# Kernel tuning notes

Measured on AMD Instinct MI355X. Metric: run time of the kernel, lower is better.

## Reference

```python
import jax, jax.numpy as jnp
import numpy as np

SOS = 0
MAX_LENGTH = 64

N_LATENTS = 256
N_CHARACTERS = 128
N_HIDDENS = 1024
BATCH = 4096


def setup_inputs() -> dict:
    key = jax.random.key(0)
    ks = jax.random.split(key, 16)
    H, L, C = N_HIDDENS, N_LATENTS, N_CHARACTERS
    s = 0.02
    return {
        "z": jax.random.normal(ks[0], (BATCH, L), dtype=jnp.float32),
        "embed_w": jax.random.normal(ks[1], (C, H), dtype=jnp.float32) * s,
        "z2h_w": jax.random.normal(ks[2], (H, L), dtype=jnp.float32) * s,
        "z2h_b": jnp.zeros((H,), dtype=jnp.float32),
        "w_ih0": jax.random.normal(ks[3], (3 * H, H + L), dtype=jnp.float32) * s,
        "w_hh0": jax.random.normal(ks[4], (3 * H, H), dtype=jnp.float32) * s,
        "b_ih0": jnp.zeros((3 * H,), dtype=jnp.float32),
        "b_hh0": jnp.zeros((3 * H,), dtype=jnp.float32),
        "w_ih1": jax.random.normal(ks[5], (3 * H, H), dtype=jnp.float32) * s,
        "w_hh1": jax.random.normal(ks[6], (3 * H, H), dtype=jnp.float32) * s,
        "b_ih1": jnp.zeros((3 * H,), dtype=jnp.float32),
        "b_hh1": jnp.zeros((3 * H,), dtype=jnp.float32),
        "h2o_w": jax.random.normal(ks[7], (C, H + L), dtype=jnp.float32) * s,
        "h2o_b": jnp.zeros((C,), dtype=jnp.float32),
    }


def _gru_cell(x, h, w_ih, w_hh, b_ih, b_hh):
    # PyTorch GRUCell math. x: [B, I], h: [B, H]
    gi = x @ w_ih.T + b_ih  # [B, 3H]
    gh = h @ w_hh.T + b_hh  # [B, 3H]
    i_r, i_z, i_n = jnp.split(gi, 3, axis=1)
    h_r, h_z, h_n = jnp.split(gh, 3, axis=1)
    r = jax.nn.sigmoid(i_r + h_r)
    zg = jax.nn.sigmoid(i_z + h_z)
    n = jnp.tanh(i_n + r * h_n)
    return (1.0 - zg) * n + zg * h


def reference(z, embed_w, z2h_w, z2h_b,
              w_ih0, w_hh0, b_ih0, b_hh0,
              w_ih1, w_hh1, b_ih1, b_hh1,
              h2o_w, h2o_b):
    batch = z.shape[0]
    h0 = z @ z2h_w.T + z2h_b  # [B, H], replicated across both GRU layers

    def step(carry, _):
        c_in, h1, h2 = carry
        e = embed_w[c_in]                      # [B, H] embedding lookup
        e = e * jax.nn.sigmoid(e)              # swish
        x = jnp.concatenate([e, z], axis=1)    # [B, H+L]
        h1 = _gru_cell(x, h1, w_ih0, w_hh0, b_ih0, b_hh0)
        h2 = _gru_cell(h1, h2, w_ih1, w_hh1, b_ih1, b_hh1)
        out = jnp.concatenate([h2, z], axis=1) @ h2o_w.T + h2o_b  # [B, C]
        # argmax(log_softmax(out)) == argmax(out)
        sample = jnp.argmax(out, axis=1).astype(jnp.int32)
        return (sample, h1, h2), out

    c0 = jnp.full((batch,), SOS, dtype=jnp.int32)
    _, outs = jax.lax.scan(step, (c0, h0, h0), None, length=MAX_LENGTH)
    return jnp.transpose(outs, (1, 0, 2))  # [B, T, C]
```

## Files before the change

kernel.cpp:

```cpp
#include <hip/hip_runtime.h>
#include <hip/hip_bf16.h>
#include <stdint.h>
#include <stddef.h>

#define B_   4096
#define H_   1024
#define L_   256
#define C_   128
#define T_   64
#define H3_  3072

typedef unsigned short u16;
typedef __attribute__((ext_vector_type(8))) short bf16x8;
typedef __attribute__((ext_vector_type(4))) float f32x4;

typedef const void __attribute__((address_space(1)))* as1_cvp;
typedef void __attribute__((address_space(3)))* as3_vp;

__device__ __forceinline__ void gl2lds16(const void* g, void* l) {
  __builtin_amdgcn_global_load_lds((as1_cvp)g, (as3_vp)l, 16, 0, 0);
}

__device__ __forceinline__ float bf2f(u16 u) {
  union { float f; unsigned int i; } x; x.i = ((unsigned int)u) << 16; return x.f;
}
__device__ __forceinline__ u16 f2bf(float f) {
  union { float f; unsigned int i; } x; x.f = f;
  unsigned int r = x.i + 0x7fffu + ((x.i >> 16) & 1u);
  return (u16)(r >> 16);
}
__device__ __forceinline__ float sigm(float x) { return 1.f / (1.f + __expf(-x)); }
__device__ __forceinline__ float tanh_fast(float x) {
  float e = __expf(2.f * x); return 1.f - 2.f / (e + 1.f);
}

template<int OUT_MODE>
__device__ __forceinline__ void gemm_tile_body(
    u16* As, u16* Ws,
    const u16* __restrict__ A, int lda,
    const u16* __restrict__ W, int ldw,
    const float* __restrict__ bias,
    void* __restrict__ C0p, void* __restrict__ C1p, int ldc, int K,
    int m0, int n0)
{
  const int tid  = threadIdx.x;
  const int wave = tid >> 6, lane = tid & 63;
  const int wm = (wave >> 1) * 64, wn = (wave & 1) * 64;
  const int lrow = lane & 15, lq = lane >> 4;
  const int arow = wave * 8 + (lane >> 3);
  const int acol = (lane & 7) * 8;

  f32x4 acc[4][4] = {};

  const u16* Ag = A + (size_t)m0 * lda;
  const u16* Wg = W + (size_t)n0 * ldw;

  for (int k0 = 0; k0 < K; k0 += 64) {
    __syncthreads();
    #pragma unroll
    for (int rd = 0; rd < 4; rd++) {
      gl2lds16(Ag + (size_t)(rd * 32 + arow) * lda + (k0 + acol), As + rd * 2048 + wave * 512);
      gl2lds16(Wg + (size_t)(rd * 32 + arow) * ldw + (k0 + acol), Ws + rd * 2048 + wave * 512);
    }
    __syncthreads();
    #pragma unroll
    for (int kk = 0; kk < 64; kk += 32) {
      bf16x8 af[4], bw[4];
      #pragma unroll
      for (int i = 0; i < 4; i++)
        af[i] = *(const bf16x8*)&As[(wm + i * 16 + lrow) * 64 + kk + lq * 8];
      #pragma unroll
      for (int j = 0; j < 4; j++)
        bw[j] = *(const bf16x8*)&Ws[(wn + j * 16 + lrow) * 64 + kk + lq * 8];
      #pragma unroll
      for (int i = 0; i < 4; i++)
        #pragma unroll
        for (int j = 0; j < 4; j++)
          acc[i][j] = __builtin_amdgcn_mfma_f32_16x16x32_bf16(af[i], bw[j], acc[i][j], 0, 0, 0);
    }
  }

  #pragma unroll
  for (int j = 0; j < 4; j++) {
    const int col = n0 + wn + j * 16 + lrow;
    const float bv = bias ? bias[col] : 0.f;
    #pragma unroll
    for (int i = 0; i < 4; i++) {
      #pragma unroll
      for (int r = 0; r < 4; r++) {
        const int row = m0 + wm + i * 16 + lq * 4 + r;
        float v = acc[i][j][r] + bv;
        if (OUT_MODE == 0) {
          ((float*)C0p)[(size_t)row * ldc + col] = v;
        } else if (OUT_MODE == 1) {
          ((u16*)C0p)[(size_t)row * ldc + col] = f2bf(v);
        } else {
          u16 hv = f2bf(v);
          ((u16*)C0p)[(size_t)row * ldc + col] = hv;
          ((u16*)C1p)[(size_t)row * ldc + col] = hv;
        }
      }
    }
  }
}

template<int OUT_MODE>
__global__ __launch_bounds__(256) void gemm_bt(
    const u16* __restrict__ A, int lda,
    const u16* __restrict__ W, int ldw,
    const float* __restrict__ bias,
    void* __restrict__ C0p, void* __restrict__ C1p, int ldc, int K)
{
  __shared__ __align__(16) u16 As[128 * 64];
  __shared__ __align__(16) u16 Ws[128 * 64];
  gemm_tile_body<OUT_MODE>(As, Ws, A, lda, W, ldw, bias, C0p, C1p, ldc, K,
                           blockIdx.y * 128, blockIdx.x * 128);
}

__device__ __forceinline__ void out_body(
    u16* As, u16* Ws, int ob,
    const u16* __restrict__ h2, const u16* __restrict__ Wo,
    const float* __restrict__ Oz, float* __restrict__ outp,
    int* __restrict__ cnew, int t)
{
  const int tid = threadIdx.x, wave = tid >> 6, lane = tid & 63;
  const int b0 = ob * 64;
  const int lrow = lane & 15, lq = lane >> 4;
  const int arow = wave * 8 + (lane >> 3);
  const int acol = (lane & 7) * 8;
  f32x4 acc[8] = {};

  for (int k0 = 0; k0 < H_; k0 += 64) {
    __syncthreads();
    #pragma unroll
    for (int rd = 0; rd < 2; rd++)
      gl2lds16(h2 + (size_t)(b0 + rd * 32 + arow) * H_ + k0 + acol, As + rd * 2048 + wave * 512);
    #pragma unroll
    for (int rd = 0; rd < 4; rd++)
      gl2lds16(Wo + (size_t)(rd * 32 + arow) * H_ + k0 + acol, Ws + rd * 2048 + wave * 512);
    __syncthreads();
    #pragma unroll
    for (int kk = 0; kk < 64; kk += 32) {
      bf16x8 af = *(const bf16x8*)&As[(wave * 16 + lrow) * 64 + kk + lq * 8];
      #pragma unroll
      for (int j = 0; j < 8; j++) {
        bf16x8 bw = *(const bf16x8*)&Ws[(j * 16 + lrow) * 64 + kk + lq * 8];
        acc[j] = __builtin_amdgcn_mfma_f32_16x16x32_bf16(af, bw, acc[j], 0, 0, 0);
      }
    }
  }

  #pragma unroll
  for (int r = 0; r < 4; r++) {
    const int row = b0 + wave * 16 + lq * 4 + r;
    float mv = -3.4e38f; int mi = 0;
    #pragma unroll
    for (int j = 0; j < 8; j++) {
      const int col = j * 16 + lrow;
      float v = acc[j][r] + Oz[(size_t)row * C_ + col];
      outp[(size_t)row * (T_ * C_) + t * C_ + col] = v;
      if (v > mv) { mv = v; mi = col; }
    }
    #pragma unroll
    for (int off = 1; off < 16; off <<= 1) {
      float ov = __shfl_xor(mv, off);
      int   oi = __shfl_xor(mi, off);
      if (ov > mv || (ov == mv && oi < mi)) { mv = ov; mi = oi; }
    }
    if (lrow == 0) cnew[row] = mi;
  }
}

__global__ __launch_bounds__(256) void out_k(
    const u16* __restrict__ h2cur, const u16* __restrict__ Wo,
    const float* __restrict__ Oz, float* __restrict__ outp,
    int* __restrict__ cbuf, int t)
{
  __shared__ __align__(16) u16 As[64 * 64];
  __shared__ __align__(16) u16 Ws[128 * 64];
  out_body(As, Ws, blockIdx.x, h2cur, Wo, Oz, outp, cbuf, t);
}


#define A_TSZ 16384
#define W_TSZ 12288

__device__ __forceinline__ void stageA_lo(const u16* Ag, int k0, u16* bA) {
  const int tid = threadIdx.x, wave = tid >> 6, lane = tid & 63;
  const int r64 = wave * 8 + (lane >> 3);
  const int cSw = (((lane & 7) ^ ((lane >> 5) << 1)) << 3);
  gl2lds16(Ag + (size_t)(r64) * H_ + k0 + cSw, bA + wave * 512);
  gl2lds16(Ag + (size_t)(64 + r64) * H_ + k0 + cSw, bA + 4096 + wave * 512);
}
__device__ __forceinline__ void stageA_hi(const u16* Ag, int k0, u16* bA) {
  const int tid = threadIdx.x, wave = tid >> 6, lane = tid & 63;
  const int r64 = wave * 8 + (lane >> 3);
  const int cSw = (((lane & 7) ^ ((lane >> 5) << 1)) << 3);
  gl2lds16(Ag + (size_t)(128 + r64) * H_ + k0 + cSw, bA + 8192 + wave * 512);
  gl2lds16(Ag + (size_t)(192 + r64) * H_ + k0 + cSw, bA + 12288 + wave * 512);
}
__device__ __forceinline__ void stageW(const u16* Wg, int k0, u16* bW) {
  const int tid = threadIdx.x, wave = tid >> 6, lane = tid & 63;
  const int r64 = wave * 8 + (lane >> 3);
  const int cSw = (((lane & 7) ^ ((lane >> 5) << 1)) << 3);
  #pragma unroll
  for (int rd = 0; rd < 3; rd++)
    gl2lds16(Wg + (size_t)(rd * 1024 + r64) * H_ + k0 + cSw, bW + rd * 4096 + wave * 512);
}

template<int PHASE>
__device__ __forceinline__ void phase_reads(const u16* bA, const u16* bW,
    bf16x8 af0[4], bf16x8 af1[4], bf16x8 bwv[2][2])
{
  const int tid = threadIdx.x, wave = tid >> 6, lane = tid & 63;
  const int wmh = wave >> 1, wj = wave & 1;
  const int lrow = lane & 15, lq = lane >> 4;
  const int rsw = ((lrow >> 2) & 1) << 4;
  const int c0 = (lq * 8) ^ rsw;
  const int c1 = (32 + lq * 8) ^ rsw;
  if (PHASE == 0) {
    #pragma unroll
    for (int i = 0; i < 4; i++)
      af0[i] = *(const bf16x8*)&bA[(wmh * 64 + i * 16 + lrow) * 64 + c0];
    #pragma unroll
    for (int u = 0; u < 2; u++) {
      bwv[0][u] = *(const bf16x8*)&bW[(wj * 32 + u * 16 + lrow) * 64 + c0];
      bwv[1][u] = *(const bf16x8*)&bW[(64 + wj * 32 + u * 16 + lrow) * 64 + c0];
    }
  } else if (PHASE == 1) {
    #pragma unroll
    for (int i = 0; i < 4; i++)
      af1[i] = *(const bf16x8*)&bA[(wmh * 64 + i * 16 + lrow) * 64 + c1];
    #pragma unroll
    for (int u = 0; u < 2; u++) {
      bwv[0][u] = *(const bf16x8*)&bW[(128 + wj * 32 + u * 16 + lrow) * 64 + c0];
      bwv[1][u] = *(const bf16x8*)&bW[(wj * 32 + u * 16 + lrow) * 64 + c1];
    }
  } else {
    #pragma unroll
    for (int u = 0; u < 2; u++) {
      bwv[0][u] = *(const bf16x8*)&bW[(64 + wj * 32 + u * 16 + lrow) * 64 + c1];
      bwv[1][u] = *(const bf16x8*)&bW[(128 + wj * 32 + u * 16 + lrow) * 64 + c1];
    }
  }
}

template<int PHASE, bool PH2v>
__device__ __forceinline__ void phase_fma(const bf16x8 bwv[2][2],
    const bf16x8 af0[4], const bf16x8 af1[4],
    f32x4 acc[3][2][4], f32x4 accN[2][4])
{
  if (PHASE == 0) {
    #pragma unroll
    for (int u = 0; u < 2; u++)
      #pragma unroll
      for (int i = 0; i < 4; i++) {
        acc[0][u][i] = __builtin_amdgcn_mfma_f32_16x16x32_bf16(af0[i], bwv[0][u], acc[0][u][i], 0, 0, 0);
        acc[1][u][i] = __builtin_amdgcn_mfma_f32_16x16x32_bf16(af0[i], bwv[1][u], acc[1][u][i], 0, 0, 0);
      }
  } else if (PHASE == 1) {
    #pragma unroll
    for (int u = 0; u < 2; u++)
      #pragma unroll
      for (int i = 0; i < 4; i++) {
        if (PH2v)
          accN[u][i] = __builtin_amdgcn_mfma_f32_16x16x32_bf16(af0[i], bwv[0][u], accN[u][i], 0, 0, 0);
        else
          acc[2][u][i] = __builtin_amdgcn_mfma_f32_16x16x32_bf16(af0[i], bwv[0][u], acc[2][u][i], 0, 0, 0);
        acc[0][u][i] = __builtin_amdgcn_mfma_f32_16x16x32_bf16(af1[i], bwv[1][u], acc[0][u][i], 0, 0, 0);
      }
  } else {
    #pragma unroll
    for (int u = 0; u < 2; u++)
      #pragma unroll
      for (int i = 0; i < 4; i++) {
        acc[1][u][i] = __builtin_amdgcn_mfma_f32_16x16x32_bf16(af1[i], bwv[0][u], acc[1][u][i], 0, 0, 0);
        if (PH2v)
          accN[u][i] = __builtin_amdgcn_mfma_f32_16x16x32_bf16(af1[i], bwv[1][u], accN[u][i], 0, 0, 0);
        else
          acc[2][u][i] = __builtin_amdgcn_mfma_f32_16x16x32_bf16(af1[i], bwv[1][u], acc[2][u][i], 0, 0, 0);
      }
  }
}

template<int NT1, int NT2, bool PH2v>
__device__ __forceinline__ void tile8(
    int v, u16* aC, u16* wC, u16* wN, u16* aN2,
    const u16* A1g, const u16* W1g, const u16* A2g, const u16* W2g,
    f32x4 acc[3][2][4], f32x4 accN[2][4])
{
  constexpr int NT = NT1 + NT2;
  if (v + 1 < NT) asm volatile("s_waitcnt vmcnt(4)" ::: "memory");
  else            asm volatile("s_waitcnt vmcnt(0)" ::: "memory");
  __builtin_amdgcn_sched_barrier(0);
  __builtin_amdgcn_s_barrier();
  __builtin_amdgcn_sched_barrier(0);

  bf16x8 af0[4], af1[4], bwv[2][2];

  phase_reads<0>(aC, wC, af0, af1, bwv);
  {
    const int w = v + 1;
    if (w < NT) {
      const u16* Wg = (w < NT1) ? W1g : W2g;
      stageW(Wg, ((w < NT1) ? w : w - NT1) * 64, wN);
    }
  }
  asm volatile("s_waitcnt lgkmcnt(0)" ::: "memory");
  __builtin_amdgcn_sched_barrier(0);
  __builtin_amdgcn_s_setprio(1);
  phase_fma<0, PH2v>(bwv, af0, af1, acc, accN);
  __builtin_amdgcn_s_setprio(0);
  __builtin_amdgcn_sched_barrier(0);
  __builtin_amdgcn_s_barrier();
  __builtin_amdgcn_sched_barrier(0);

  phase_reads<1>(aC, wC, af0, af1, bwv);
  {
    const int w = v + 2;
    if (w < NT) {
      const u16* Ag = (w < NT1) ? A1g : A2g;
      stageA_lo(Ag, ((w < NT1) ? w : w - NT1) * 64, aN2);
    }
  }
  asm volatile("s_waitcnt lgkmcnt(0)" ::: "memory");
  __builtin_amdgcn_sched_barrier(0);
  __builtin_amdgcn_s_setprio(1);
  phase_fma<1, PH2v>(bwv, af0, af1, acc, accN);
  __builtin_amdgcn_s_setprio(0);
  __builtin_amdgcn_sched_barrier(0);
  __builtin_amdgcn_s_barrier();
  __builtin_amdgcn_sched_barrier(0);

  phase_reads<2>(aC, wC, af0, af1, bwv);
  {
    const int w = v + 2;
    if (w < NT) {
      const u16* Ag = (w < NT1) ? A1g : A2g;
      stageA_hi(Ag, ((w < NT1) ? w : w - NT1) * 64, aN2);
    }
  }
  asm volatile("s_waitcnt lgkmcnt(0)" ::: "memory");
  __builtin_amdgcn_sched_barrier(0);
  __builtin_amdgcn_s_setprio(1);
  phase_fma<2, PH2v>(bwv, af0, af1, acc, accN);
  __builtin_amdgcn_s_setprio(0);
  __builtin_amdgcn_sched_barrier(0);
}

template<int NT1, int NT2>
__device__ __forceinline__ void kloop8(
    u16* As, u16* Ws,
    const u16* A1g, const u16* W1g, const u16* A2g, const u16* W2g,
    f32x4 acc[3][2][4], f32x4 accN[2][4])
{
  constexpr int NT = NT1 + NT2;
  u16* aB0 = As; u16* aB1 = As + A_TSZ; u16* aB2 = As + 2 * A_TSZ;
  u16* wB0 = Ws; u16* wB1 = Ws + W_TSZ;

  stageA_lo(A1g, 0, aB0); stageA_hi(A1g, 0, aB0);
  stageW(W1g, 0, wB0);
  if (NT > 1) {
    const u16* Ag = (1 < NT1) ? A1g : A2g;
    const int k0 = (1 < NT1) ? 64 : 0;
    stageA_lo(Ag, k0, aB1); stageA_hi(Ag, k0, aB1);
  }

  u16* aC = aB0; u16* aN1 = aB1; u16* aN2 = aB2;
  u16* wC = wB0; u16* wN = wB1;

  #pragma unroll 1
  for (int v = 0; v < NT1; v++) {
    tile8<NT1, NT2, false>(v, aC, wC, wN, aN2, A1g, W1g, A2g, W2g, acc, accN);
    u16* t = aC; aC = aN1; aN1 = aN2; aN2 = t;
    u16* tw = wC; wC = wN; wN = tw;
  }
  #pragma unroll 1
  for (int v = NT1; v < NT; v++) {
    tile8<NT1, NT2, true>(v, aC, wC, wN, aN2, A1g, W1g, A2g, W2g, acc, accN);
    u16* t = aC; aC = aN1; aN1 = aN2; aN2 = t;
    u16* tw = wC; wC = wN; wN = tw;
  }
}

__global__ __launch_bounds__(512, 2) void gru0_256(
    const u16* __restrict__ h1old, const u16* __restrict__ whh0,
    const float* __restrict__ b_hh0, const int* __restrict__ cbuf,
    const u16* __restrict__ Egi, const u16* __restrict__ Gz,
    u16* __restrict__ h1new)
{
  __shared__ __align__(16) u16 As[3 * A_TSZ];
  __shared__ __align__(16) u16 Ws[2 * W_TSZ];
  const int bid = blockIdx.x;
  const int xcd = bid & 7, k = bid >> 3;
  const int jt = xcd * 2 + (k & 1);
  const int m  = k >> 1;
  const int m0 = m * 256, j0 = jt * 64;

  f32x4 acc[3][2][4] = {};
  f32x4 accN[2][4] = {};
  kloop8<16, 0>(As, Ws,
                h1old + (size_t)m0 * H_, whh0 + (size_t)j0 * H_,
                h1old + (size_t)m0 * H_, whh0 + (size_t)j0 * H_,
                acc, accN);

  const int tid = threadIdx.x, wave = tid >> 6, lane = tid & 63;
  const int wmh = wave >> 1, wj = wave & 1;
  const int lrow = lane & 15, lq = lane >> 4;

  #pragma unroll
  for (int u = 0; u < 2; u++) {
    const int j = j0 + wj * 32 + u * 16 + lrow;
    const float bR = b_hh0[j];
    const float bZ = b_hh0[H_ + j];
    const float bN = b_hh0[2 * H_ + j];
    #pragma unroll
    for (int i = 0; i < 4; i++) {
      #pragma unroll
      for (int rr = 0; rr < 4; rr++) {
        const int row = m0 + wmh * 64 + i * 16 + lq * 4 + rr;
        const size_t eb = (size_t)cbuf[row] * H3_ + j;
        const size_t gb = (size_t)row * H3_ + j;
        float r  = sigm(bf2f(Egi[eb])           + bf2f(Gz[gb])           + acc[0][u][i][rr] + bR);
        float zg = sigm(bf2f(Egi[eb + H_])      + bf2f(Gz[gb + H_])      + acc[1][u][i][rr] + bZ);
        float nn = tanh_fast(bf2f(Egi[eb + 2 * H_]) + bf2f(Gz[gb + 2 * H_])
                             + r * (acc[2][u][i][rr] + bN));
        float hold = bf2f(h1old[(size_t)row * H_ + j]);
        h1new[(size_t)row * H_ + j] = f2bf((1.f - zg) * nn + zg * hold);
      }
    }
  }
}

__global__ __launch_bounds__(512, 2) void gru1_256(
    const u16* __restrict__ h1, const u16* __restrict__ h2old,
    const u16* __restrict__ wih1, const u16* __restrict__ whh1,
    const float* __restrict__ b_ih1, const float* __restrict__ b_hh1,
    u16* __restrict__ h2new)
{
  __shared__ __align__(16) u16 As[3 * A_TSZ];
  __shared__ __align__(16) u16 Ws[2 * W_TSZ];
  const int bid = blockIdx.x;
  const int xcd = bid & 7, k = bid >> 3;
  const int jt = xcd * 2 + (k & 1);
  const int m  = k >> 1;
  const int m0 = m * 256, j0 = jt * 64;

  f32x4 acc[3][2][4] = {};
  f32x4 accN[2][4] = {};
  kloop8<16, 16>(As, Ws,
                 h1    + (size_t)m0 * H_, wih1 + (size_t)j0 * H_,
                 h2old + (size_t)m0 * H_, whh1 + (size_t)j0 * H_,
                 acc, accN);

  const int tid = threadIdx.x, wave = tid >> 6, lane = tid & 63;
  const int wmh = wave >> 1, wj = wave & 1;
  const int lrow = lane & 15, lq = lane >> 4;

  #pragma unroll
  for (int u = 0; u < 2; u++) {
    const int j = j0 + wj * 32 + u * 16 + lrow;
    const float bR  = b_ih1[j] + b_hh1[j];
    const float bZ  = b_ih1[H_ + j] + b_hh1[H_ + j];
    const float bNi = b_ih1[2 * H_ + j];
    const float bNh = b_hh1[2 * H_ + j];
    #pragma unroll
    for (int i = 0; i < 4; i++) {
      #pragma unroll
      for (int rr = 0; rr < 4; rr++) {
        const int row = m0 + wmh * 64 + i * 16 + lq * 4 + rr;
        float r  = sigm(acc[0][u][i][rr] + bR);
        float zg = sigm(acc[1][u][i][rr] + bZ);
        float nn = tanh_fast(acc[2][u][i][rr] + bNi + r * (accN[u][i][rr] + bNh));
        float hold = bf2f(h2old[(size_t)row * H_ + j]);
        h2new[(size_t)row * H_ + j] = f2bf((1.f - zg) * nn + zg * hold);
      }
    }
  }
}

__global__ __launch_bounds__(256) void conv_bf16_k(const float* __restrict__ s, u16* __restrict__ d, int n) {
  int i = blockIdx.x * 256 + threadIdx.x;
  if (i < n) d[i] = f2bf(s[i]);
}
__global__ __launch_bounds__(256) void conv_split_k(const float* __restrict__ s, u16* __restrict__ dA,
                                                    u16* __restrict__ dZ, int rows) {
  int i = blockIdx.x * 256 + threadIdx.x;
  if (i >= rows * 1280) return;
  int rr = i / 1280, col = i - rr * 1280;
  float v = s[i];
  if (col < 1024) dA[(size_t)rr * 1024 + col] = f2bf(v);
  else            dZ[(size_t)rr * 256 + (col - 1024)] = f2bf(v);
}
__global__ __launch_bounds__(256) void conv_swish_k(const float* __restrict__ s, u16* __restrict__ d, int n) {
  int i = blockIdx.x * 256 + threadIdx.x;
  if (i < n) { float e = s[i]; d[i] = f2bf(e * sigm(e)); }
}

static inline char* wsal(char*& p, size_t bytes) {
  char* r = p; p += (bytes + 255) & ~(size_t)255; return r;
}

extern "C" void kernel_launch(void* const* d_in, const int* in_sizes, int n_in,
                              void* d_out, int out_size, void* d_ws, size_t ws_size,
                              hipStream_t stream) {
  const float* z       = (const float*)d_in[0];
  const float* embed_w = (const float*)d_in[1];
  const float* z2h_w   = (const float*)d_in[2];
  const float* z2h_b   = (const float*)d_in[3];
  const float* w_ih0   = (const float*)d_in[4];
  const float* w_hh0   = (const float*)d_in[5];
  const float* b_ih0   = (const float*)d_in[6];
  const float* b_hh0   = (const float*)d_in[7];
  const float* w_ih1   = (const float*)d_in[8];
  const float* w_hh1   = (const float*)d_in[9];
  const float* b_ih1   = (const float*)d_in[10];
  const float* b_hh1   = (const float*)d_in[11];
  const float* h2o_w   = (const float*)d_in[12];
  const float* h2o_b   = (const float*)d_in[13];
  float* outp = (float*)d_out;

  char* p = (char*)d_ws;
  u16* whh0  = (u16*)wsal(p, (size_t)H3_ * H_ * 2);
  u16* wih1  = (u16*)wsal(p, (size_t)H3_ * H_ * 2);
  u16* whh1  = (u16*)wsal(p, (size_t)H3_ * H_ * 2);
  u16* wih0a = (u16*)wsal(p, (size_t)H3_ * H_ * 2);
  u16* wih0z = (u16*)wsal(p, (size_t)H3_ * L_ * 2);
  u16* h2oa  = (u16*)wsal(p, (size_t)C_ * H_ * 2);
  u16* h2oz  = (u16*)wsal(p, (size_t)C_ * L_ * 2);
  u16* z2hb  = (u16*)wsal(p, (size_t)H_ * L_ * 2);
  u16* zb    = (u16*)wsal(p, (size_t)B_ * L_ * 2);
  u16* swe   = (u16*)wsal(p, (size_t)C_ * H_ * 2);
  u16* EgiB  = (u16*)wsal(p, (size_t)C_ * H3_ * 2);
  u16* Gz    = (u16*)wsal(p, (size_t)B_ * H3_ * 2);
  float* Oz  = (float*)wsal(p, (size_t)B_ * C_ * 4);
  u16* h1a   = (u16*)wsal(p, (size_t)B_ * H_ * 2);
  u16* h1b   = (u16*)wsal(p, (size_t)B_ * H_ * 2);
  u16* h2a   = (u16*)wsal(p, (size_t)B_ * H_ * 2);
  u16* h2b   = (u16*)wsal(p, (size_t)B_ * H_ * 2);
  int* cbuf  = (int*)wsal(p, (size_t)B_ * 4);

  conv_bf16_k<<<(B_*L_ + 255)/256, 256, 0, stream>>>(z, zb, B_*L_);
  conv_bf16_k<<<(H_*L_ + 255)/256, 256, 0, stream>>>(z2h_w, z2hb, H_*L_);
  conv_bf16_k<<<(H3_*H_ + 255)/256, 256, 0, stream>>>(w_hh0, whh0, H3_*H_);
  conv_bf16_k<<<(H3_*H_ + 255)/256, 256, 0, stream>>>(w_ih1, wih1, H3_*H_);
  conv_bf16_k<<<(H3_*H_ + 255)/256, 256, 0, stream>>>(w_hh1, whh1, H3_*H_);
  conv_split_k<<<(H3_*1280 + 255)/256, 256, 0, stream>>>(w_ih0, wih0a, wih0z, H3_);
  conv_split_k<<<(C_*1280 + 255)/256, 256, 0, stream>>>(h2o_w, h2oa, h2oz, C_);
  conv_swish_k<<<(C_*H_ + 255)/256, 256, 0, stream>>>(embed_w, swe, C_*H_);
  hipMemsetAsync(cbuf, 0, B_ * sizeof(int), stream);

  gemm_bt<2><<<dim3(H_/128, B_/128), 256, 0, stream>>>(zb, L_, z2hb, L_, z2h_b, h1a, h2a, H_, L_);
  gemm_bt<1><<<dim3(H3_/128, 1), 256, 0, stream>>>(swe, H_, wih0a, H_, b_ih0, EgiB, nullptr, H3_, H_);
  gemm_bt<1><<<dim3(H3_/128, B_/128), 256, 0, stream>>>(zb, L_, wih0z, L_, nullptr, Gz, nullptr, H3_, L_);
  gemm_bt<0><<<dim3(1, B_/128), 256, 0, stream>>>(zb, L_, h2oz, L_, h2o_b, Oz, nullptr, C_, L_);

  for (int t = 0; t < T_; t++) {
    const u16* h2cur = (t & 1) ? h2b : h2a;
    u16*       h2nxt = (t & 1) ? h2a : h2b;
    const u16* h1cur = (t & 1) ? h1b : h1a;
    u16*       h1nxt = (t & 1) ? h1a : h1b;
    if (t > 0)
      out_k<<<64, 256, 0, stream>>>(h2cur, h2oa, Oz, outp, cbuf, t - 1);
    gru0_256<<<256, 512, 0, stream>>>(h1cur, whh0, b_hh0, cbuf, EgiB, Gz, h1nxt);
    gru1_256<<<256, 512, 0, stream>>>(h1nxt, h2cur, wih1, whh1, b_ih1, b_hh1, h2nxt);
  }
  out_k<<<64, 256, 0, stream>>>(h2a, h2oa, Oz, outp, cbuf, T_ - 1);
}
```

Baseline: 7.143 ms.

## Double-buffer output projection loads and hoist all GRU tile LDS reads

```diff
diff --git a/kernel.cpp b/kernel.cpp
--- a/kernel.cpp
+++ b/kernel.cpp
@@ -117,6 +117,22 @@
                            blockIdx.y * 128, blockIdx.x * 128);
 }
 
+#define OA_TSZ 4096
+#define OW_TSZ 8192
+
+__device__ __forceinline__ void o_stage(const u16* h2, const u16* Wo,
+                                        int b0, int k0, u16* bA, u16* bW) {
+  const int tid = threadIdx.x, wave = tid >> 6, lane = tid & 63;
+  const int arow = wave * 8 + (lane >> 3);
+  const int cSw = (((lane & 7) ^ ((lane >> 5) << 1)) << 3);
+  #pragma unroll
+  for (int rd = 0; rd < 2; rd++)
+    gl2lds16(h2 + (size_t)(b0 + rd * 32 + arow) * H_ + k0 + cSw, bA + rd * 2048 + wave * 512);
+  #pragma unroll
+  for (int rd = 0; rd < 4; rd++)
+    gl2lds16(Wo + (size_t)(rd * 32 + arow) * H_ + k0 + cSw, bW + rd * 2048 + wave * 512);
+}
+
 __device__ __forceinline__ void out_body(
     u16* As, u16* Ws, int ob,
     const u16* __restrict__ h2, const u16* __restrict__ Wo,
@@ -126,28 +142,35 @@
   const int tid = threadIdx.x, wave = tid >> 6, lane = tid & 63;
   const int b0 = ob * 64;
   const int lrow = lane & 15, lq = lane >> 4;
-  const int arow = wave * 8 + (lane >> 3);
-  const int acol = (lane & 7) * 8;
+  const int rsw = ((lrow >> 2) & 1) << 4;
   f32x4 acc[8] = {};
 
-  for (int k0 = 0; k0 < H_; k0 += 64) {
-    __syncthreads();
-    #pragma unroll
-    for (int rd = 0; rd < 2; rd++)
-      gl2lds16(h2 + (size_t)(b0 + rd * 32 + arow) * H_ + k0 + acol, As + rd * 2048 + wave * 512);
-    #pragma unroll
-    for (int rd = 0; rd < 4; rd++)
-      gl2lds16(Wo + (size_t)(rd * 32 + arow) * H_ + k0 + acol, Ws + rd * 2048 + wave * 512);
-    __syncthreads();
+  o_stage(h2, Wo, b0, 0, As, Ws);
+  o_stage(h2, Wo, b0, 64, As + OA_TSZ, Ws + OW_TSZ);
+
+  #pragma unroll 1
+  for (int v = 0; v < 16; v++) {
+    u16* bA = (v & 1) ? As + OA_TSZ : As;
+    u16* bW = (v & 1) ? Ws + OW_TSZ : Ws;
+    if (v + 1 < 16) asm volatile("s_waitcnt vmcnt(6)" ::: "memory");
+    else            asm volatile("s_waitcnt vmcnt(0)" ::: "memory");
+    __builtin_amdgcn_sched_barrier(0);
+    __builtin_amdgcn_s_barrier();
+    __builtin_amdgcn_sched_barrier(0);
     #pragma unroll
     for (int kk = 0; kk < 64; kk += 32) {
-      bf16x8 af = *(const bf16x8*)&As[(wave * 16 + lrow) * 64 + kk + lq * 8];
+      const int c = (kk + lq * 8) ^ rsw;
+      bf16x8 af = *(const bf16x8*)&bA[(wave * 16 + lrow) * 64 + c];
       #pragma unroll
       for (int j = 0; j < 8; j++) {
-        bf16x8 bw = *(const bf16x8*)&Ws[(j * 16 + lrow) * 64 + kk + lq * 8];
+        bf16x8 bw = *(const bf16x8*)&bW[(j * 16 + lrow) * 64 + c];
         acc[j] = __builtin_amdgcn_mfma_f32_16x16x32_bf16(af, bw, acc[j], 0, 0, 0);
       }
     }
+    __builtin_amdgcn_sched_barrier(0);
+    __builtin_amdgcn_s_barrier();
+    __builtin_amdgcn_sched_barrier(0);
+    if (v + 2 < 16) o_stage(h2, Wo, b0, (v + 2) * 64, bA, bW);
   }
 
   #pragma unroll
@@ -176,8 +199,8 @@
     const float* __restrict__ Oz, float* __restrict__ outp,
     int* __restrict__ cbuf, int t)
 {
-  __shared__ __align__(16) u16 As[64 * 64];
-  __shared__ __align__(16) u16 Ws[128 * 64];
+  __shared__ __align__(16) u16 As[2 * OA_TSZ];
+  __shared__ __align__(16) u16 Ws[2 * OW_TSZ];
   out_body(As, Ws, blockIdx.x, h2cur, Wo, Oz, outp, cbuf, t);
 }
 
@@ -208,9 +231,9 @@
     gl2lds16(Wg + (size_t)(rd * 1024 + r64) * H_ + k0 + cSw, bW + rd * 4096 + wave * 512);
 }
 
-template<int PHASE>
-__device__ __forceinline__ void phase_reads(const u16* bA, const u16* bW,
-    bf16x8 af0[4], bf16x8 af1[4], bf16x8 bwv[2][2])
+__device__ __forceinline__ void tile_reads(const u16* bA, const u16* bW,
+    bf16x8 af0[4], bf16x8 af1[4],
+    bf16x8 bw0[2][2], bf16x8 bw1[2][2], bf16x8 bw2[2][2])
 {
   const int tid = threadIdx.x, wave = tid >> 6, lane = tid & 63;
   const int wmh = wave >> 1, wj = wave & 1;
@@ -218,30 +241,26 @@
   const int rsw = ((lrow >> 2) & 1) << 4;
   const int c0 = (lq * 8) ^ rsw;
   const int c1 = (32 + lq * 8) ^ rsw;
-  if (PHASE == 0) {
-    #pragma unroll
-    for (int i = 0; i < 4; i++)
-      af0[i] = *(const bf16x8*)&bA[(wmh * 64 + i * 16 + lrow) * 64 + c0];
-    #pragma unroll
-    for (int u = 0; u < 2; u++) {
-      bwv[0][u] = *(const bf16x8*)&bW[(wj * 32 + u * 16 + lrow) * 64 + c0];
-      bwv[1][u] = *(const bf16x8*)&bW[(64 + wj * 32 + u * 16 + lrow) * 64 + c0];
-    }
-  } else if (PHASE == 1) {
-    #pragma unroll
-    for (int i = 0; i < 4; i++)
-      af1[i] = *(const bf16x8*)&bA[(wmh * 64 + i * 16 + lrow) * 64 + c1];
-    #pragma unroll
-    for (int u = 0; u < 2; u++) {
-      bwv[0][u] = *(const bf16x8*)&bW[(128 + wj * 32 + u * 16 + lrow) * 64 + c0];
-      bwv[1][u] = *(const bf16x8*)&bW[(wj * 32 + u * 16 + lrow) * 64 + c1];
-    }
-  } else {
-    #pragma unroll
-    for (int u = 0; u < 2; u++) {
-      bwv[0][u] = *(const bf16x8*)&bW[(64 + wj * 32 + u * 16 + lrow) * 64 + c1];
-      bwv[1][u] = *(const bf16x8*)&bW[(128 + wj * 32 + u * 16 + lrow) * 64 + c1];
-    }
+  #pragma unroll
+  for (int i = 0; i < 4; i++)
+    af0[i] = *(const bf16x8*)&bA[(wmh * 64 + i * 16 + lrow) * 64 + c0];
+  #pragma unroll
+  for (int u = 0; u < 2; u++) {
+    bw0[0][u] = *(const bf16x8*)&bW[(wj * 32 + u * 16 + lrow) * 64 + c0];
+    bw0[1][u] = *(const bf16x8*)&bW[(64 + wj * 32 + u * 16 + lrow) * 64 + c0];
+  }
+  #pragma unroll
+  for (int i = 0; i < 4; i++)
+    af1[i] = *(const bf16x8*)&bA[(wmh * 64 + i * 16 + lrow) * 64 + c1];
+  #pragma unroll
+  for (int u = 0; u < 2; u++) {
+    bw1[0][u] = *(const bf16x8*)&bW[(128 + wj * 32 + u * 16 + lrow) * 64 + c0];
+    bw1[1][u] = *(const bf16x8*)&bW[(wj * 32 + u * 16 + lrow) * 64 + c1];
+  }
+  #pragma unroll
+  for (int u = 0; u < 2; u++) {
+    bw2[0][u] = *(const bf16x8*)&bW[(64 + wj * 32 + u * 16 + lrow) * 64 + c1];
+    bw2[1][u] = *(const bf16x8*)&bW[(128 + wj * 32 + u * 16 + lrow) * 64 + c1];
   }
 }
 
@@ -284,7 +303,7 @@
 }
 
 template<int NT1, int NT2, bool PH2v>
-__device__ __forceinline__ void tile8(
+__device__ __forceinline__ void tile_p(
     int v, u16* aC, u16* wC, u16* wN, u16* aN2,
     const u16* A1g, const u16* W1g, const u16* A2g, const u16* W2g,
     f32x4 acc[3][2][4], f32x4 accN[2][4])
@@ -296,54 +315,37 @@
   __builtin_amdgcn_s_barrier();
   __builtin_amdgcn_sched_barrier(0);
 
-  bf16x8 af0[4], af1[4], bwv[2][2];
-
-  phase_reads<0>(aC, wC, af0, af1, bwv);
+  bf16x8 af0[4], af1[4], bw0[2][2], bw1[2][2], bw2[2][2];
+  tile_reads(aC, wC, af0, af1, bw0, bw1, bw2);
+
   {
     const int w = v + 1;
-    if (w < NT) {
-      const u16* Wg = (w < NT1) ? W1g : W2g;
-      stageW(Wg, ((w < NT1) ? w : w - NT1) * 64, wN);
-    }
-  }
-  asm volatile("s_waitcnt lgkmcnt(0)" ::: "memory");
-  __builtin_amdgcn_sched_barrier(0);
+    if (w < NT) stageW((w < NT1) ? W1g : W2g, ((w < NT1) ? w : w - NT1) * 64, wN);
+  }
   __builtin_amdgcn_s_setprio(1);
-  phase_fma<0, PH2v>(bwv, af0, af1, acc, accN);
+  phase_fma<0, PH2v>(bw0, af0, af1, acc, accN);
   __builtin_amdgcn_s_setprio(0);
   __builtin_amdgcn_sched_barrier(0);
   __builtin_amdgcn_s_barrier();
   __builtin_amdgcn_sched_barrier(0);
 
-  phase_reads<1>(aC, wC, af0, af1, bwv);
   {
     const int w = v + 2;
-    if (w < NT) {
-      const u16* Ag = (w < NT1) ? A1g : A2g;
-      stageA_lo(Ag, ((w < NT1) ? w : w - NT1) * 64, aN2);
-    }
-  }
-  asm volatile("s_waitcnt lgkmcnt(0)" ::: "memory");
-  __builtin_amdgcn_sched_barrier(0);
+    if (w < NT) stageA_lo((w < NT1) ? A1g : A2g, ((w < NT1) ? w : w - NT1) * 64, aN2);
+  }
   __builtin_amdgcn_s_setprio(1);
-  phase_fma<1, PH2v>(bwv, af0, af1, acc, accN);
+  phase_fma<1, PH2v>(bw1, af0, af1, acc, accN);
   __builtin_amdgcn_s_setprio(0);
   __builtin_amdgcn_sched_barrier(0);
   __builtin_amdgcn_s_barrier();
   __builtin_amdgcn_sched_barrier(0);
 
-  phase_reads<2>(aC, wC, af0, af1, bwv);
   {
     const int w = v + 2;
-    if (w < NT) {
-      const u16* Ag = (w < NT1) ? A1g : A2g;
-      stageA_hi(Ag, ((w < NT1) ? w : w - NT1) * 64, aN2);
-    }
-  }
-  asm volatile("s_waitcnt lgkmcnt(0)" ::: "memory");
-  __builtin_amdgcn_sched_barrier(0);
+    if (w < NT) stageA_hi((w < NT1) ? A1g : A2g, ((w < NT1) ? w : w - NT1) * 64, aN2);
+  }
   __builtin_amdgcn_s_setprio(1);
-  phase_fma<2, PH2v>(bwv, af0, af1, acc, accN);
+  phase_fma<2, PH2v>(bw2, af0, af1, acc, accN);
   __builtin_amdgcn_s_setprio(0);
   __builtin_amdgcn_sched_barrier(0);
 }
@@ -371,13 +373,13 @@
 
   #pragma unroll 1
   for (int v = 0; v < NT1; v++) {
-    tile8<NT1, NT2, false>(v, aC, wC, wN, aN2, A1g, W1g, A2g, W2g, acc, accN);
+    tile_p<NT1, NT2, false>(v, aC, wC, wN, aN2, A1g, W1g, A2g, W2g, acc, accN);
     u16* t = aC; aC = aN1; aN1 = aN2; aN2 = t;
     u16* tw = wC; wC = wN; wN = tw;
   }
   #pragma unroll 1
   for (int v = NT1; v < NT; v++) {
-    tile8<NT1, NT2, true>(v, aC, wC, wN, aN2, A1g, W1g, A2g, W2g, acc, accN);
+    tile_p<NT1, NT2, true>(v, aC, wC, wN, aN2, A1g, W1g, A2g, W2g, acc, accN);
     u16* t = aC; aC = aN1; aN1 = aN2; aN2 = t;
     u16* tw = wC; wC = wN; wN = tw;
   }
```

New measurement: 7.409 ms. 3.7% more time.
